# Kernel tuning notes

Hardware: AMD Instinct MI355X
Metric: run time of the kernel (lower is better)

## Reference

```python
import jax, jax.numpy as jnp
import numpy as np

NUM_CLASSES = 10
GAMMA = 1.0
EPS = 1e-12


def setup_inputs() -> dict:
    key = jax.random.key(0)
    k1, k2, k3, k4 = jax.random.split(key, 4)
    x = jax.random.normal(k1, (1024, 64), dtype=jnp.float32)
    exemplars = jax.random.normal(k2, (50000, 64), dtype=jnp.float32)
    exemplar_labels = jax.random.randint(k3, (50000,), 0, NUM_CLASSES)
    # beta_raw initialized as softplus^{-1}(init_beta) with init_beta=1.0
    init_beta = 1.0
    beta_raw = jnp.array([np.log(np.exp(init_beta) - 1.0)], dtype=jnp.float32)
    return {"x": x, "exemplars": exemplars, "exemplar_labels": exemplar_labels,
            "beta_raw": beta_raw}


def reference(x, exemplars, exemplar_labels, beta_raw):
    # Squared Euclidean distances (weight_diag == ones) via GEMM expansion:
    # d2[b, e] = ||x_b||^2 + ||e_e||^2 - 2 <x_b, e_e>
    x2 = jnp.sum(x * x, axis=-1, keepdims=True)            # (B, 1)
    e2 = jnp.sum(exemplars * exemplars, axis=-1)           # (Ne,)
    d2 = x2 + e2[None, :] - 2.0 * (x @ exemplars.T)        # (B, Ne)
    d2 = jnp.maximum(d2, 0.0)  # true sq-dist is nonneg; guards GEMM round-off
    beta = jax.nn.softplus(beta_raw[0])
    sims = jnp.exp(-beta * d2)                              # (B, Ne)
    # scatter-add similarities into per-class bins: (C, B) -> (B, C)
    class_sims = jax.ops.segment_sum(sims.T, exemplar_labels,
                                     num_segments=NUM_CLASSES).T
    logits = GAMMA * jnp.log(class_sims + EPS)
    return logits
```

## Files before the change

kernel.cpp:

```cpp
#include <hip/hip_runtime.h>


#define NB      1024
#define NE      50000
#define NE_PAD  50176
#define NCHUNK  196
#define CROWS   256
#define KD      64
#define NC      10
#define SROWS   64
#define NSTAGE  4
#define LROW    72

using half8   = __attribute__((ext_vector_type(8))) _Float16;
using half4v  = __attribute__((ext_vector_type(4))) _Float16;
using floatx4 = __attribute__((ext_vector_type(4))) float;

__device__ __forceinline__ float softplus_f(float x) {
  return (x > 20.f) ? x : log1pf(__expf(x));
}

__global__ __launch_bounds__(256) void prep_kernel(
    const float* __restrict__ x, const float* __restrict__ ex,
    const int* __restrict__ labels, const float* __restrict__ beta_raw,
    _Float16* __restrict__ ex_h, float* __restrict__ ce,
    _Float16* __restrict__ x_h, float* __restrict__ cb,
    int* __restrict__ lab_pad)
{
  const int tid = threadIdx.x;
  const float beta = softplus_f(beta_raw[0]);

  const int row = blockIdx.x * 16 + (tid >> 4);
  const int l16 = tid & 15;

  if (row < NE_PAD) {
    float4 v = make_float4(0.f, 0.f, 0.f, 0.f);
    if (row < NE) v = ((const float4*)ex)[row * 16 + l16];
    half4v hv = { (_Float16)v.x, (_Float16)v.y, (_Float16)v.z, (_Float16)v.w };
    *(half4v*)(ex_h + (size_t)row * KD + l16 * 4) = hv;
    float s = v.x*v.x + v.y*v.y + v.z*v.z + v.w*v.w;
    #pragma unroll
    for (int m = 1; m < 16; m <<= 1) s += __shfl_xor(s, m, 64);
    if (l16 == 0) ce[row] = (row < NE) ? (-beta * s) : -1e30f;
    if (l16 == 1) lab_pad[row] = (row < NE) ? labels[row] : 0;
  } else {
    const int rx = row - NE_PAD;
    float4 v = ((const float4*)x)[rx * 16 + l16];
    half4v hv = { (_Float16)v.x, (_Float16)v.y, (_Float16)v.z, (_Float16)v.w };
    *(half4v*)(x_h + (size_t)rx * KD + l16 * 4) = hv;
    float s = v.x*v.x + v.y*v.y + v.z*v.z + v.w*v.w;
    #pragma unroll
    for (int m = 1; m < 16; m <<= 1) s += __shfl_xor(s, m, 64);
    if (l16 == 0) cb[rx] = -beta * s;
  }
}

__global__ __launch_bounds__(256) void main_kernel(
    const _Float16* __restrict__ ex_h, const float* __restrict__ ce,
    const _Float16* __restrict__ x_h, const float* __restrict__ cb,
    const int* __restrict__ lab_pad, const float* __restrict__ beta_raw,
    float* __restrict__ part)
{
  __shared__ _Float16 Ah[2][SROWS * LROW];
  __shared__ float    Ce[2][SROWS];
  __shared__ int      Lb[2][SROWS];

  const int tid  = threadIdx.x;
  const int wave = tid >> 6;
  const int lane = tid & 63;
  const int l15  = lane & 15;
  const int quad = lane >> 4;

  const int btile = blockIdx.x;
  const int chunk = blockIdx.y;
  const int e0    = chunk * CROWS;
  const int bm    = btile * 64 + wave * 16;

  const float beta = softplus_f(beta_raw[0]);
  const float s2 = 2.f * beta;

  const half8* xrow = (const half8*)(x_h + (size_t)(bm + l15) * KD);
  const half8 bx0 = xrow[quad];
  const half8 bx1 = xrow[quad + 4];
  const float cbl = cb[bm + l15];

  const int srow = tid >> 2;
  const int scol = tid & 3;
  const _Float16* gsrc = ex_h + (size_t)(e0 + srow) * KD + scol * 16;
  const int lofs = srow * LROW + scol * 16;

  half8 pr0 = *(const half8*)(gsrc);
  half8 pr1 = *(const half8*)(gsrc + 8);
  float prc = 0.f; int prl = 0;
  if (wave == 0) prc = ce[e0 + lane];
  if (wave == 1) prl = lab_pad[e0 + lane];

  *(half8*)(&Ah[0][lofs])     = pr0;
  *(half8*)(&Ah[0][lofs + 8]) = pr1;
  if (wave == 0) Ce[0][lane] = prc;
  if (wave == 1) Lb[0][lane] = prl;
  __syncthreads();

  floatx4 acc = {0.f, 0.f, 0.f, 0.f};

  #pragma unroll
  for (int st = 0; st < NSTAGE; ++st) {
    const int b = st & 1;

    if (st + 1 < NSTAGE) {
      const _Float16* g = gsrc + (size_t)(st + 1) * SROWS * KD;
      pr0 = *(const half8*)(g);
      pr1 = *(const half8*)(g + 8);
      if (wave == 0) prc = ce[e0 + (st + 1) * SROWS + lane];
      if (wave == 1) prl = lab_pad[e0 + (st + 1) * SROWS + lane];
    }

    #pragma unroll
    for (int sub = 0; sub < 4; ++sub) {
      const int abase = (sub * 16 + l15) * LROW + quad * 8;
      const half8 ae0 = *(const half8*)(&Ah[b][abase]);
      const half8 ae1 = *(const half8*)(&Ah[b][abase + 32]);
      const float4 ce4 = *(const float4*)(&Ce[b][sub * 16 + quad * 4]);
      const int4   lb4 = *(const int4*)(&Lb[b][sub * 16 + quad * 4]);

      floatx4 d = {0.f, 0.f, 0.f, 0.f};
      d = __builtin_amdgcn_mfma_f32_16x16x32_f16(ae0, bx0, d, 0, 0, 0);
      d = __builtin_amdgcn_mfma_f32_16x16x32_f16(ae1, bx1, d, 0, 0, 0);

      const float cef[4] = { ce4.x, ce4.y, ce4.z, ce4.w };
      half4v p;
      #pragma unroll
      for (int r = 0; r < 4; ++r) {
        const float t = fminf(fmaf(s2, d[r], cbl + cef[r]), 0.f);
        p[r] = (_Float16)__expf(t);
      }

      half4v oh;
      oh[0] = (lb4.x == l15) ? (_Float16)1.f : (_Float16)0.f;
      oh[1] = (lb4.y == l15) ? (_Float16)1.f : (_Float16)0.f;
      oh[2] = (lb4.z == l15) ? (_Float16)1.f : (_Float16)0.f;
      oh[3] = (lb4.w == l15) ? (_Float16)1.f : (_Float16)0.f;

      acc = __builtin_amdgcn_mfma_f32_16x16x16f16(oh, p, acc, 0, 0, 0);
    }

    if (st + 1 < NSTAGE) {
      __syncthreads();
      const int nb = (st + 1) & 1;
      *(half8*)(&Ah[nb][lofs])     = pr0;
      *(half8*)(&Ah[nb][lofs + 8]) = pr1;
      if (wave == 0) Ce[nb][lane] = prc;
      if (wave == 1) Lb[nb][lane] = prl;
      __syncthreads();
    }
  }

  float* dst = part + (size_t)chunk * (NB * NC);
  #pragma unroll
  for (int r = 0; r < 4; ++r) {
    const int c = quad * 4 + r;
    if (c < NC) {
      dst[(bm + l15) * NC + c] = acc[r];
    }
  }
}

__global__ __launch_bounds__(256) void reduce_kernel(
    const float* __restrict__ part, float* __restrict__ out)
{
  const int bc = blockIdx.x * 256 + threadIdx.x;
  if (bc < NB * NC) {
    float s = 0.f;
    #pragma unroll 7
    for (int k = 0; k < NCHUNK; ++k) s += part[(size_t)k * (NB * NC) + bc];
    out[bc] = __logf(s + 1e-12f);
  }
}

extern "C" void kernel_launch(void* const* d_in, const int* in_sizes, int n_in,
                              void* d_out, int out_size, void* d_ws, size_t ws_size,
                              hipStream_t stream)
{
  const float* x        = (const float*)d_in[0];
  const float* ex       = (const float*)d_in[1];
  const int*   labels   = (const int*)d_in[2];
  const float* beta_raw = (const float*)d_in[3];
  float* out = (float*)d_out;

  char* ws = (char*)d_ws;
  _Float16* ex_h    = (_Float16*)ws;
  float*    ce      = (float*)(ws + 6422528);
  _Float16* x_h     = (_Float16*)(ws + 6623232);
  float*    cb      = (float*)(ws + 6754304);
  int*      lab_pad = (int*)(ws + 6758400);
  float*    part    = (float*)(ws + 6959104);

  prep_kernel<<<3200, 256, 0, stream>>>(x, ex, labels, beta_raw,
                                        ex_h, ce, x_h, cb, lab_pad);
  dim3 g(16, 196);
  main_kernel<<<g, 256, 0, stream>>>(ex_h, ce, x_h, cb, lab_pad, beta_raw, part);
  reduce_kernel<<<40, 256, 0, stream>>>(part, out);
}
```

Measured before the change: 107.1 us.

## Double per-wave batch tile, swizzle LDS, precompute one-hot label fragments

Each wave now handles 32 query rows instead of 16. This halves the grid along the batch axis and reuses each exemplar tile from LDS for twice as many MFMAs. The LDS padding is replaced by an XOR swizzle, and the Ce/label staging through shared memory is removed. The one-hot label fragments are now built once in the prep kernel and read directly from global memory along with ce. The cost is more registers and fewer blocks, and the tail of the padded labels is handled by clamping the read index.

Measured after the change: 108.1 us. About the same (+0.9%).

```diff
diff --git a/kernel.cpp b/kernel.cpp
--- a/kernel.cpp
+++ b/kernel.cpp
@@ -10,7 +10,6 @@
 #define NC      10
 #define SROWS   64
 #define NSTAGE  4
-#define LROW    72
 
 using half8   = __attribute__((ext_vector_type(8))) _Float16;
 using half4v  = __attribute__((ext_vector_type(4))) _Float16;
@@ -25,7 +24,7 @@
     const int* __restrict__ labels, const float* __restrict__ beta_raw,
     _Float16* __restrict__ ex_h, float* __restrict__ ce,
     _Float16* __restrict__ x_h, float* __restrict__ cb,
-    int* __restrict__ lab_pad)
+    _Float16* __restrict__ oh_pre)
 {
   const int tid = threadIdx.x;
   const float beta = softplus_f(beta_raw[0]);
@@ -42,7 +41,6 @@
     #pragma unroll
     for (int m = 1; m < 16; m <<= 1) s += __shfl_xor(s, m, 64);
     if (l16 == 0) ce[row] = (row < NE) ? (-beta * s) : -1e30f;
-    if (l16 == 1) lab_pad[row] = (row < NE) ? labels[row] : 0;
   } else {
     const int rx = row - NE_PAD;
     float4 v = ((const float4*)x)[rx * 16 + l16];
@@ -53,17 +51,28 @@
     for (int m = 1; m < 16; m <<= 1) s += __shfl_xor(s, m, 64);
     if (l16 == 0) cb[rx] = -beta * s;
   }
+
+  if (blockIdx.x < (NE_PAD / 16) && tid < 64) {
+    const int l15  = tid & 15;
+    const int quad = tid >> 4;
+    const int base = min(blockIdx.x * 16 + quad * 4, NE - 4);
+    const int4 lb = *(const int4*)(labels + base);
+    half4v oh;
+    oh[0] = (lb.x == l15) ? (_Float16)1.f : (_Float16)0.f;
+    oh[1] = (lb.y == l15) ? (_Float16)1.f : (_Float16)0.f;
+    oh[2] = (lb.z == l15) ? (_Float16)1.f : (_Float16)0.f;
+    oh[3] = (lb.w == l15) ? (_Float16)1.f : (_Float16)0.f;
+    ((half4v*)oh_pre)[blockIdx.x * 64 + tid] = oh;
+  }
 }
 
 __global__ __launch_bounds__(256) void main_kernel(
     const _Float16* __restrict__ ex_h, const float* __restrict__ ce,
     const _Float16* __restrict__ x_h, const float* __restrict__ cb,
-    const int* __restrict__ lab_pad, const float* __restrict__ beta_raw,
+    const _Float16* __restrict__ oh_pre, const float* __restrict__ beta_raw,
     float* __restrict__ part)
 {
-  __shared__ _Float16 Ah[2][SROWS * LROW];
-  __shared__ float    Ce[2][SROWS];
-  __shared__ int      Lb[2][SROWS];
+  __shared__ _Float16 Ah[2][SROWS * KD];
 
   const int tid  = threadIdx.x;
   const int wave = tid >> 6;
@@ -74,34 +83,37 @@
   const int btile = blockIdx.x;
   const int chunk = blockIdx.y;
   const int e0    = chunk * CROWS;
-  const int bm    = btile * 64 + wave * 16;
+  const int bm    = btile * 128 + wave * 32;
 
   const float beta = softplus_f(beta_raw[0]);
   const float s2 = 2.f * beta;
 
-  const half8* xrow = (const half8*)(x_h + (size_t)(bm + l15) * KD);
-  const half8 bx0 = xrow[quad];
-  const half8 bx1 = xrow[quad + 4];
-  const float cbl = cb[bm + l15];
+  const half8* xr0 = (const half8*)(x_h + (size_t)(bm + l15) * KD);
+  const half8* xr1 = (const half8*)(x_h + (size_t)(bm + 16 + l15) * KD);
+  const half8 bx00 = xr0[quad];
+  const half8 bx01 = xr0[quad + 4];
+  const half8 bx10 = xr1[quad];
+  const half8 bx11 = xr1[quad + 4];
+  const float cbl0 = cb[bm + l15];
+  const float cbl1 = cb[bm + 16 + l15];
 
   const int srow = tid >> 2;
   const int scol = tid & 3;
+  const int ssw  = srow & 7;
   const _Float16* gsrc = ex_h + (size_t)(e0 + srow) * KD + scol * 16;
-  const int lofs = srow * LROW + scol * 16;
+  const int lofs0 = srow * KD + (((2 * scol)     ^ ssw) * 8);
+  const int lofs1 = srow * KD + (((2 * scol + 1) ^ ssw) * 8);
 
   half8 pr0 = *(const half8*)(gsrc);
   half8 pr1 = *(const half8*)(gsrc + 8);
-  float prc = 0.f; int prl = 0;
-  if (wave == 0) prc = ce[e0 + lane];
-  if (wave == 1) prl = lab_pad[e0 + lane];
-
-  *(half8*)(&Ah[0][lofs])     = pr0;
-  *(half8*)(&Ah[0][lofs + 8]) = pr1;
-  if (wave == 0) Ce[0][lane] = prc;
-  if (wave == 1) Lb[0][lane] = prl;
+  *(half8*)(&Ah[0][lofs0]) = pr0;
+  *(half8*)(&Ah[0][lofs1]) = pr1;
   __syncthreads();
 
-  floatx4 acc = {0.f, 0.f, 0.f, 0.f};
+  floatx4 acc0 = {0.f, 0.f, 0.f, 0.f};
+  floatx4 acc1 = {0.f, 0.f, 0.f, 0.f};
+
+  const int rsw = l15 & 7;
 
   #pragma unroll
   for (int st = 0; st < NSTAGE; ++st) {
@@ -111,46 +123,48 @@
       const _Float16* g = gsrc + (size_t)(st + 1) * SROWS * KD;
       pr0 = *(const half8*)(g);
       pr1 = *(const half8*)(g + 8);
-      if (wave == 0) prc = ce[e0 + (st + 1) * SROWS + lane];
-      if (wave == 1) prl = lab_pad[e0 + (st + 1) * SROWS + lane];
-    }
-
+    }
+
+    float4 ce4s[4]; half4v ohs[4];
     #pragma unroll
     for (int sub = 0; sub < 4; ++sub) {
-      const int abase = (sub * 16 + l15) * LROW + quad * 8;
-      const half8 ae0 = *(const half8*)(&Ah[b][abase]);
-      const half8 ae1 = *(const half8*)(&Ah[b][abase + 32]);
-      const float4 ce4 = *(const float4*)(&Ce[b][sub * 16 + quad * 4]);
-      const int4   lb4 = *(const int4*)(&Lb[b][sub * 16 + quad * 4]);
-
-      floatx4 d = {0.f, 0.f, 0.f, 0.f};
-      d = __builtin_amdgcn_mfma_f32_16x16x32_f16(ae0, bx0, d, 0, 0, 0);
-      d = __builtin_amdgcn_mfma_f32_16x16x32_f16(ae1, bx1, d, 0, 0, 0);
-
+      ce4s[sub] = *(const float4*)(ce + e0 + st * SROWS + sub * 16 + quad * 4);
+      ohs[sub]  = ((const half4v*)oh_pre)[(size_t)(chunk * 16 + st * 4 + sub) * 64 + lane];
+    }
+
+    #pragma unroll
+    for (int sub = 0; sub < 4; ++sub) {
+      const int rs = sub * 16 + l15;
+      const half8 ae0 = *(const half8*)(&Ah[b][rs * KD + ((quad ^ rsw) * 8)]);
+      const half8 ae1 = *(const half8*)(&Ah[b][rs * KD + (((quad + 4) ^ rsw) * 8)]);
+
+      floatx4 d0 = {0.f, 0.f, 0.f, 0.f};
+      d0 = __builtin_amdgcn_mfma_f32_16x16x32_f16(ae0, bx00, d0, 0, 0, 0);
+      d0 = __builtin_amdgcn_mfma_f32_16x16x32_f16(ae1, bx01, d0, 0, 0, 0);
+      floatx4 d1 = {0.f, 0.f, 0.f, 0.f};
+      d1 = __builtin_amdgcn_mfma_f32_16x16x32_f16(ae0, bx10, d1, 0, 0, 0);
+      d1 = __builtin_amdgcn_mfma_f32_16x16x32_f16(ae1, bx11, d1, 0, 0, 0);
+
+      const float4 ce4 = ce4s[sub];
       const float cef[4] = { ce4.x, ce4.y, ce4.z, ce4.w };
-      half4v p;
+      half4v p0, p1;
       #pragma unroll
       for (int r = 0; r < 4; ++r) {
-        const float t = fminf(fmaf(s2, d[r], cbl + cef[r]), 0.f);
-        p[r] = (_Float16)__expf(t);
+        const float t0 = fminf(fmaf(s2, d0[r], cbl0 + cef[r]), 0.f);
+        const float t1 = fminf(fmaf(s2, d1[r], cbl1 + cef[r]), 0.f);
+        p0[r] = (_Float16)__expf(t0);
+        p1[r] = (_Float16)__expf(t1);
       }
 
-      half4v oh;
-      oh[0] = (lb4.x == l15) ? (_Float16)1.f : (_Float16)0.f;
-      oh[1] = (lb4.y == l15) ? (_Float16)1.f : (_Float16)0.f;
-      oh[2] = (lb4.z == l15) ? (_Float16)1.f : (_Float16)0.f;
-      oh[3] = (lb4.w == l15) ? (_Float16)1.f : (_Float16)0.f;
-
-      acc = __builtin_amdgcn_mfma_f32_16x16x16f16(oh, p, acc, 0, 0, 0);
+      acc0 = __builtin_amdgcn_mfma_f32_16x16x16f16(ohs[sub], p0, acc0, 0, 0, 0);
+      acc1 = __builtin_amdgcn_mfma_f32_16x16x16f16(ohs[sub], p1, acc1, 0, 0, 0);
     }
 
     if (st + 1 < NSTAGE) {
       __syncthreads();
       const int nb = (st + 1) & 1;
-      *(half8*)(&Ah[nb][lofs])     = pr0;
-      *(half8*)(&Ah[nb][lofs + 8]) = pr1;
-      if (wave == 0) Ce[nb][lane] = prc;
-      if (wave == 1) Lb[nb][lane] = prl;
+      *(half8*)(&Ah[nb][lofs0]) = pr0;
+      *(half8*)(&Ah[nb][lofs1]) = pr1;
       __syncthreads();
     }
   }
@@ -160,7 +174,8 @@
   for (int r = 0; r < 4; ++r) {
     const int c = quad * 4 + r;
     if (c < NC) {
-      dst[(bm + l15) * NC + c] = acc[r];
+      dst[(bm + l15) * NC + c]      = acc0[r];
+      dst[(bm + 16 + l15) * NC + c] = acc1[r];
     }
   }
 }
@@ -188,16 +203,16 @@
   float* out = (float*)d_out;
 
   char* ws = (char*)d_ws;
-  _Float16* ex_h    = (_Float16*)ws;
-  float*    ce      = (float*)(ws + 6422528);
-  _Float16* x_h     = (_Float16*)(ws + 6623232);
-  float*    cb      = (float*)(ws + 6754304);
-  int*      lab_pad = (int*)(ws + 6758400);
-  float*    part    = (float*)(ws + 6959104);
+  _Float16* ex_h   = (_Float16*)ws;
+  float*    ce     = (float*)(ws + 6422528);
+  _Float16* x_h    = (_Float16*)(ws + 6623232);
+  float*    cb     = (float*)(ws + 6754304);
+  _Float16* oh_pre = (_Float16*)(ws + 6758400);
+  float*    part   = (float*)(ws + 8364032);
 
   prep_kernel<<<3200, 256, 0, stream>>>(x, ex, labels, beta_raw,
-                                        ex_h, ce, x_h, cb, lab_pad);
-  dim3 g(16, 196);
-  main_kernel<<<g, 256, 0, stream>>>(ex_h, ce, x_h, cb, lab_pad, beta_raw, part);
+                                        ex_h, ce, x_h, cb, oh_pre);
+  dim3 g(8, 196);
+  main_kernel<<<g, 256, 0, stream>>>(ex_h, ce, x_h, cb, oh_pre, beta_raw, part);
   reduce_kernel<<<40, 256, 0, stream>>>(part, out);
 }
```
